# Performance work log

Measured on AMD Instinct MI355X. Metric: run time of the kernel, lower is better.

Reference implementation:

```python
import jax, jax.numpy as jnp
import numpy as np

H, W, SCALE = 480, 640, 8  # full-res grid and coarse downsample factor (hw0_i/hw0_c)


def _struct_feats(pts, anchor_ids):
    """pts: [N, H*W, 3]; anchor_ids: [N, A] int -> [N, L, 4*A] with L=(H//SCALE)*(W//SCALE)."""
    N = pts.shape[0]
    coarse = pts.reshape(N, H, W, 3)[:, ::SCALE, ::SCALE, :].reshape(N, -1, 3)  # [N, L, 3]
    anchors = jnp.take_along_axis(pts, anchor_ids[:, :, None], axis=1)          # [N, A, 3]
    diff = coarse[:, :, None, :] - anchors[:, None, :, :]                        # [N, L, A, 3]
    dist = jnp.sum(diff * diff, axis=-1, keepdims=True)                          # [N, L, A, 1]
    s = jnp.concatenate([diff, dist], axis=-1)                                   # [N, L, A, 4]
    s = s / jnp.sum(jnp.abs(s), axis=-2, keepdims=True)                          # L1 norm over anchor axis
    s = jnp.swapaxes(s, -1, -2).reshape(N, coarse.shape[1], -1)                  # [N, L, 4A]
    return s


def _mlp(x, W1, b1, W2, b2):
    return jax.nn.relu(x @ W1 + b1) @ W2 + b2


def setup_inputs() -> dict:
    key = jax.random.key(0)
    ks = jax.random.split(key, 10)
    N, L, C, A, P = 4, 4800, 256, 128, H * W
    D = C + 4 * A  # 768
    return {
        "feat0": jax.random.normal(ks[0], (N, L, C), jnp.float32),
        "feat1": jax.random.normal(ks[1], (N, L, C), jnp.float32),
        "pts_3d0": jax.random.normal(ks[2], (N, P, 3), jnp.float32),
        "pts_3d1": jax.random.normal(ks[3], (N, P, 3), jnp.float32),
        "anchor_i_ids": jax.random.randint(ks[4], (N, A), 0, P),
        "anchor_j_ids": jax.random.randint(ks[5], (N, A), 0, P),
        "W1": jax.random.normal(ks[6], (D, D), jnp.float32) * (1.0 / np.sqrt(D)),
        "b1": jnp.zeros((D,), jnp.float32),
        "W2": jax.random.normal(ks[7], (D, C), jnp.float32) * (1.0 / np.sqrt(D)),
        "b2": jnp.zeros((C,), jnp.float32),
    }


def reference(feat0, feat1, pts_3d0, pts_3d1, anchor_i_ids, anchor_j_ids, W1, b1, W2, b2):
    s0 = _struct_feats(pts_3d0, anchor_i_ids)  # [N, L, 4A]
    s1 = _struct_feats(pts_3d1, anchor_j_ids)
    aug0 = _mlp(jnp.concatenate([feat0, s0], axis=-1), W1, b1, W2, b2)  # [N, L, C]
    aug1 = _mlp(jnp.concatenate([feat1, s1], axis=-1), W1, b1, W2, b2)
    return (aug0, aug1)
```

## Files before the change

### kernel.cpp

```cpp
#include <hip/hip_runtime.h>
#include <stdint.h>
#include <stddef.h>

typedef __attribute__((ext_vector_type(8))) short short8;
typedef __attribute__((ext_vector_type(4))) short short4v;
typedef __attribute__((ext_vector_type(4))) float f32x4;

typedef const __attribute__((address_space(3))) char* lds_cp;

#define GLDS16(gp, lp)                                                        \
    __builtin_amdgcn_global_load_lds(                                         \
        (const __attribute__((address_space(1))) void*)(gp),                  \
        (__attribute__((address_space(3))) void*)(lp), 16, 0, 0)

__device__ __forceinline__ short8 ldsr16(lds_cp p) {
    short8 v;
    asm volatile("ds_read_b128 %0, %1" : "=v"(v) : "v"(p));
    return v;
}

template <int N>
__device__ __forceinline__ void wait_lgkm() {
    static_assert(N == 0 || N == 2 || N == 4 || N == 8, "unsupported count");
    if constexpr (N == 0) asm volatile("s_waitcnt lgkmcnt(0)" ::: "memory");
    else if constexpr (N == 2) asm volatile("s_waitcnt lgkmcnt(2)" ::: "memory");
    else if constexpr (N == 4) asm volatile("s_waitcnt lgkmcnt(4)" ::: "memory");
    else if constexpr (N == 8) asm volatile("s_waitcnt lgkmcnt(8)" ::: "memory");
    __builtin_amdgcn_sched_barrier(0);
}

template <int N>
__device__ __forceinline__ void wait_vm() {
    static_assert(N == 0 || N == 2 || N == 4, "unsupported count");
    if constexpr (N == 0) asm volatile("s_waitcnt vmcnt(0)" ::: "memory");
    else if constexpr (N == 2) asm volatile("s_waitcnt vmcnt(2)" ::: "memory");
    else if constexpr (N == 4) asm volatile("s_waitcnt vmcnt(4)" ::: "memory");
}

__device__ __forceinline__ unsigned short f2bf(float f) {
    union { float f; uint32_t u; } v;
    v.f = f;
    uint32_t u = v.u;
    u += 0x7FFFu + ((u >> 16) & 1u);
    return (unsigned short)(u >> 16);
}

__global__ __launch_bounds__(1024) void transpose_w(
    const float* __restrict__ W1, const float* __restrict__ W2,
    unsigned short* __restrict__ w1t, unsigned short* __restrict__ w2t)
{
    __shared__ float tile[32][33];
    int b = blockIdx.x;
    const float* src; unsigned short* dst; int R, C, bx, by;
    if (b < 576) { src = W1; dst = w1t; R = 768; C = 768; bx = b % 24; by = b / 24; }
    else { b -= 576; src = W2; dst = w2t; R = 768; C = 256; bx = b % 8; by = b / 8; }
    const int c0 = bx * 32, r0 = by * 32;
    const int tx = threadIdx.x, ty = threadIdx.y;
    tile[ty][tx] = src[(size_t)(r0 + ty) * C + (c0 + tx)];
    __syncthreads();
    dst[(size_t)(c0 + ty) * R + (r0 + tx)] = f2bf(tile[tx][ty]);
}

__global__ __launch_bounds__(256) void struct_pack(
    const float* __restrict__ feat0, const float* __restrict__ feat1,
    const float* __restrict__ pts0,  const float* __restrict__ pts1,
    const int* __restrict__ ids0,    const int* __restrict__ ids1,
    unsigned short* __restrict__ xw)
{
    const int m = blockIdx.x * 4 + (threadIdx.x >> 6);
    const int t = m / 19200;
    const int r = m % 19200;
    const int n = r / 4800;
    const int l = r % 4800;
    const float* feat = t ? feat1 : feat0;
    const float* pts  = (t ? pts1 : pts0) + (size_t)n * (307200 * 3);
    const int*   ids  = (t ? ids1 : ids0) + n * 128;
    const int a = threadIdx.x & 63;

    const int lr = l / 80, lc = l % 80;
    const int p  = (lr * 8) * 640 + lc * 8;
    const float cx = pts[p * 3 + 0], cy = pts[p * 3 + 1], cz = pts[p * 3 + 2];

    const int id0 = ids[a], id1 = ids[a + 64];
    const float d0x = cx - pts[id0 * 3 + 0];
    const float d0y = cy - pts[id0 * 3 + 1];
    const float d0z = cz - pts[id0 * 3 + 2];
    const float d0d = d0x * d0x + d0y * d0y + d0z * d0z;
    const float d1x = cx - pts[id1 * 3 + 0];
    const float d1y = cy - pts[id1 * 3 + 1];
    const float d1z = cz - pts[id1 * 3 + 2];
    const float d1d = d1x * d1x + d1y * d1y + d1z * d1z;

    float p0 = fabsf(d0x) + fabsf(d1x);
    float p1 = fabsf(d0y) + fabsf(d1y);
    float p2 = fabsf(d0z) + fabsf(d1z);
    float p3 = d0d + d1d;
#pragma unroll
    for (int off = 32; off; off >>= 1) {
        p0 += __shfl_xor(p0, off);
        p1 += __shfl_xor(p1, off);
        p2 += __shfl_xor(p2, off);
        p3 += __shfl_xor(p3, off);
    }
    const float i0 = 1.0f / p0, i1 = 1.0f / p1, i2 = 1.0f / p2, i3 = 1.0f / p3;

    unsigned short* xrow = xw + (size_t)m * 768;
    const float* frow = feat + (size_t)(n * 4800 + l) * 256;
    const float4 fv = ((const float4*)frow)[a];
    short4v s4;
    s4.x = (short)f2bf(fv.x); s4.y = (short)f2bf(fv.y);
    s4.z = (short)f2bf(fv.z); s4.w = (short)f2bf(fv.w);
    *(short4v*)(xrow + a * 4) = s4;

    xrow[256 + 0 * 128 + a]      = f2bf(d0x * i0);
    xrow[256 + 0 * 128 + a + 64] = f2bf(d1x * i0);
    xrow[256 + 1 * 128 + a]      = f2bf(d0y * i1);
    xrow[256 + 1 * 128 + a + 64] = f2bf(d1y * i1);
    xrow[256 + 2 * 128 + a]      = f2bf(d0z * i2);
    xrow[256 + 2 * 128 + a + 64] = f2bf(d1z * i2);
    xrow[256 + 3 * 128 + a]      = f2bf(d0d * i3);
    xrow[256 + 3 * 128 + a + 64] = f2bf(d1d * i3);
}

template <int MI, int NJ, int WRN_LOG, bool RELU, bool OUT_BF16>
__global__ __launch_bounds__(512, 2) void gemm_t(
    const unsigned short* __restrict__ A,
    const unsigned short* __restrict__ Bt,
    const float* __restrict__ bias,
    void* __restrict__ Cout,
    int K, int N, int ntx, int q8, int r8)
{
    constexpr int WRN = 1 << WRN_LOG;
    constexpr int WRM = 8 / WRN;
    constexpr int BM = WRM * MI * 16;
    constexpr int BN = WRN * NJ * 16;
    constexpr int ASLOT = BM * 128;
    constexpr int BSLOT = BN * 128;
    constexpr int ALD = BM / 64;
    constexpr int BLD = BN / 64;

    extern __shared__ char lds[];
    char* ldsB = lds + 3 * ASLOT;
    const int nt = K >> 6;

    const int bid = blockIdx.x;
    const int xcd = bid & 7, idx = bid >> 3;
    const int w = (xcd < r8 ? xcd * (q8 + 1) : r8 * (q8 + 1) + (xcd - r8) * q8) + idx;
    const int n0 = (w % ntx) * BN;
    const int m0 = (w / ntx) * BM;

    const int tid = threadIdx.x;
    const int lane = tid & 63;
    const int wv = tid >> 6;
    const int wr = wv >> WRN_LOG;
    const int wc = wv & (WRN - 1);

    const int slr = lane >> 3;
    const int kc  = (lane & 7) ^ slr;
    const unsigned short* gA = A  + (size_t)(m0 + wv * 8 + slr) * K + kc * 8;
    const unsigned short* gB = Bt + (size_t)(n0 + wv * 8 + slr) * K + kc * 8;

    auto stA = [&](int slot, int i, int kt) {
        GLDS16(gA + (size_t)i * 64 * K + kt, lds + slot * ASLOT + (i * 64 + wv * 8) * 128);
    };
    auto stB = [&](int slot, int j, int kt) {
        GLDS16(gB + (size_t)j * 64 * K + kt, ldsB + slot * BSLOT + (j * 64 + wv * 8) * 128);
    };

    const int rsel = lane & 15;
    const int kbh  = lane >> 4;
    const int ck0 = ((kbh) ^ (rsel & 7)) * 16;
    const int ck1 = ((4 + kbh) ^ (rsel & 7)) * 16;
    const int aRowB = (wr * (MI * 16) + rsel) * 128;
    const int bRowB = (wc * (NJ * 16) + rsel) * 128;

    auto LDA = [&](int slot, int mi, int ks) -> short8 {
        return ldsr16((lds_cp)(lds + slot * ASLOT + aRowB + mi * 2048 + (ks ? ck1 : ck0)));
    };
    auto LDB = [&](int slot, int nj, int ks) -> short8 {
        return ldsr16((lds_cp)(ldsB + slot * BSLOT + bRowB + nj * 2048 + (ks ? ck1 : ck0)));
    };

    f32x4 acc[MI][NJ] = {};
    short8 aL[MI / 2], aH[MI / 2], aL1[MI / 2], aH1[MI / 2], bF0[NJ], bF1[NJ];

    {
#pragma unroll
        for (int i = 0; i < ALD; ++i) stA(0, i, 0);
#pragma unroll
        for (int j = 0; j < BLD; ++j) stB(0, j, 0);
        if (nt > 1) {
#pragma unroll
            for (int i = 0; i < ALD; ++i) stA(1, i, 64);
            wait_vm<ALD>();
        } else {
            wait_vm<0>();
        }
        __builtin_amdgcn_s_barrier();
    }

    int cb3 = 0;
    for (int t = 0; t < nt; ++t) {
        const int cb2 = t & 1;
        const int sb2 = cb2 ^ 1;
        int sa3 = cb3 + 2; if (sa3 >= 3) sa3 -= 3;
        const int kt1 = (t + 1) << 6;
        const int kt2 = (t + 2) << 6;
        const bool stb = (t + 1) < nt;
        const bool sta = (t + 2) < nt;

#pragma unroll
        for (int nj = 0; nj < NJ; ++nj) bF0[nj] = LDB(cb2, nj, 0);
#pragma unroll
        for (int mi = 0; mi < MI / 2; ++mi) aL[mi] = LDA(cb3, mi, 0);
#pragma unroll
        for (int mi = 0; mi < MI / 2; ++mi) aH[mi] = LDA(cb3, MI / 2 + mi, 0);

        wait_lgkm<MI / 2>();
        __builtin_amdgcn_s_setprio(1);
#pragma unroll
        for (int mi = 0; mi < MI / 2; ++mi)
#pragma unroll
            for (int nj = 0; nj < NJ; ++nj)
                acc[mi][nj] = __builtin_amdgcn_mfma_f32_16x16x32_bf16(aL[mi], bF0[nj], acc[mi][nj], 0, 0, 0);
        __builtin_amdgcn_s_setprio(0);

#pragma unroll
        for (int nj = 0; nj < NJ; ++nj) bF1[nj] = LDB(cb2, nj, 1);
        if (stb) {
#pragma unroll
            for (int j = 0; j < BLD; ++j) stB(sb2, j, kt1);
        }

        wait_lgkm<NJ>();
        __builtin_amdgcn_s_setprio(1);
#pragma unroll
        for (int mi = 0; mi < MI / 2; ++mi)
#pragma unroll
            for (int nj = 0; nj < NJ; ++nj)
                acc[MI / 2 + mi][nj] = __builtin_amdgcn_mfma_f32_16x16x32_bf16(aH[mi], bF0[nj], acc[MI / 2 + mi][nj], 0, 0, 0);
        __builtin_amdgcn_s_setprio(0);

#pragma unroll
        for (int mi = 0; mi < MI / 2; ++mi) aL1[mi] = LDA(cb3, mi, 1);
#pragma unroll
        for (int mi = 0; mi < MI / 2; ++mi) aH1[mi] = LDA(cb3, MI / 2 + mi, 1);
        if (sta) {
#pragma unroll
            for (int i = 0; i < ALD; ++i) stA(sa3, i, kt2);
        }

        wait_lgkm<MI / 2>();
        __builtin_amdgcn_s_setprio(1);
#pragma unroll
        for (int mi = 0; mi < MI / 2; ++mi)
#pragma unroll
            for (int nj = 0; nj < NJ; ++nj)
                acc[mi][nj] = __builtin_amdgcn_mfma_f32_16x16x32_bf16(aL1[mi], bF1[nj], acc[mi][nj], 0, 0, 0);
        __builtin_amdgcn_s_setprio(0);

        wait_lgkm<0>();
        __builtin_amdgcn_s_setprio(1);
#pragma unroll
        for (int mi = 0; mi < MI / 2; ++mi)
#pragma unroll
            for (int nj = 0; nj < NJ; ++nj)
                acc[MI / 2 + mi][nj] = __builtin_amdgcn_mfma_f32_16x16x32_bf16(aH1[mi], bF1[nj], acc[MI / 2 + mi][nj], 0, 0, 0);
        __builtin_amdgcn_s_setprio(0);

        if (t + 1 < nt) {
            if (sta) wait_vm<ALD>();
            else     wait_vm<0>();
            __builtin_amdgcn_s_barrier();
        }
        cb3 = (cb3 + 1 == 3) ? 0 : cb3 + 1;
    }

    const int crow = (lane >> 4) * 4;
    const int ccol = lane & 15;
#pragma unroll
    for (int nj = 0; nj < NJ; ++nj) {
        const int col = n0 + wc * (NJ * 16) + nj * 16 + ccol;
        const float bv = bias[col];
#pragma unroll
        for (int mi = 0; mi < MI; ++mi) {
#pragma unroll
            for (int rg = 0; rg < 4; ++rg) {
                const int row = m0 + wr * (MI * 16) + mi * 16 + crow + rg;
                float v = acc[mi][nj][rg] + bv;
                if (RELU) v = fmaxf(v, 0.0f);
                if (OUT_BF16) {
                    ((unsigned short*)Cout)[(size_t)row * N + col] = f2bf(v);
                } else {
                    ((float*)Cout)[(size_t)row * N + col] = v;
                }
            }
        }
    }
}

extern "C" void kernel_launch(void* const* d_in, const int* in_sizes, int n_in,
                              void* d_out, int out_size, void* d_ws, size_t ws_size,
                              hipStream_t stream) {
    const float* feat0 = (const float*)d_in[0];
    const float* feat1 = (const float*)d_in[1];
    const float* pts0  = (const float*)d_in[2];
    const float* pts1  = (const float*)d_in[3];
    const int*   ids0  = (const int*)d_in[4];
    const int*   ids1  = (const int*)d_in[5];
    const float* W1    = (const float*)d_in[6];
    const float* b1    = (const float*)d_in[7];
    const float* W2    = (const float*)d_in[8];
    const float* b2    = (const float*)d_in[9];
    float* out = (float*)d_out;

    char* ws = (char*)d_ws;
    unsigned short* xw  = (unsigned short*)(ws);
    unsigned short* h   = (unsigned short*)(ws + 58982400);
    unsigned short* w1t = (unsigned short*)(ws + 117964800);
    unsigned short* w2t = (unsigned short*)(ws + 119144448);

    const int LDS1 = 3 * 32768 + 2 * 32768;
    const int LDS2 = 3 * 16384 + 2 * 16384;
    (void)hipFuncSetAttribute((const void*)&gemm_t<8, 4, 2, true, true>,
                              hipFuncAttributeMaxDynamicSharedMemorySize, LDS1);
    (void)hipFuncSetAttribute((const void*)&gemm_t<4, 2, 2, false, false>,
                              hipFuncAttributeMaxDynamicSharedMemorySize, LDS2);

    transpose_w<<<768, dim3(32, 32), 0, stream>>>(W1, W2, w1t, w2t);

    struct_pack<<<9600, 256, 0, stream>>>(feat0, feat1, pts0, pts1, ids0, ids1, xw);

    gemm_t<8, 4, 2, true, true><<<450, 512, LDS1, stream>>>(xw, w1t, b1, (void*)h, 768, 768, 3, 56, 2);
    gemm_t<4, 2, 2, false, false><<<600, 512, LDS2, stream>>>(h, w2t, b2, (void*)out, 768, 256, 2, 75, 0);
}
```

Baseline: 112.9 us.

## Add 256x128 pipelined GEMM kernel with A-fragment prefetch for first MLP layer

Replaces the first-layer GEMM (768x768 with ReLU and bf16 output) with a new kernel that uses 256x128 tiles instead of 256x256, doubling the grid to 900 blocks. The kernel keeps a three-stage global-to-LDS ring for both A and B and prefetches the next K-step's A fragments into registers while the current MFMAs run. LDS reads are interleaved with MFMA groups using fine-grained lgkmcnt waits and s_setprio. Smaller tiles cut per-block LDS and even out the work across CUs, at the cost of reloading A more often and holding more registers.

```diff
diff --git a/kernel.cpp b/kernel.cpp
--- a/kernel.cpp
+++ b/kernel.cpp
@@ -21,20 +21,22 @@
 
 template <int N>
 __device__ __forceinline__ void wait_lgkm() {
-    static_assert(N == 0 || N == 2 || N == 4 || N == 8, "unsupported count");
     if constexpr (N == 0) asm volatile("s_waitcnt lgkmcnt(0)" ::: "memory");
     else if constexpr (N == 2) asm volatile("s_waitcnt lgkmcnt(2)" ::: "memory");
     else if constexpr (N == 4) asm volatile("s_waitcnt lgkmcnt(4)" ::: "memory");
     else if constexpr (N == 8) asm volatile("s_waitcnt lgkmcnt(8)" ::: "memory");
+    else if constexpr (N == 10) asm volatile("s_waitcnt lgkmcnt(10)" ::: "memory");
+    else if constexpr (N == 12) asm volatile("s_waitcnt lgkmcnt(12)" ::: "memory");
+    else static_assert(N == 0, "unsupported count");
     __builtin_amdgcn_sched_barrier(0);
 }
 
 template <int N>
 __device__ __forceinline__ void wait_vm() {
-    static_assert(N == 0 || N == 2 || N == 4, "unsupported count");
     if constexpr (N == 0) asm volatile("s_waitcnt vmcnt(0)" ::: "memory");
     else if constexpr (N == 2) asm volatile("s_waitcnt vmcnt(2)" ::: "memory");
     else if constexpr (N == 4) asm volatile("s_waitcnt vmcnt(4)" ::: "memory");
+    else static_assert(N == 0, "unsupported count");
 }
 
 __device__ __forceinline__ unsigned short f2bf(float f) {
@@ -120,6 +122,202 @@
     xrow[256 + 2 * 128 + a + 64] = f2bf(d1z * i2);
     xrow[256 + 3 * 128 + a]      = f2bf(d0d * i3);
     xrow[256 + 3 * 128 + a + 64] = f2bf(d1d * i3);
+}
+
+template <bool RELU, bool OUT_BF16>
+__global__ __launch_bounds__(512, 2) void gemm_p(
+    const unsigned short* __restrict__ A,
+    const unsigned short* __restrict__ Bt,
+    const float* __restrict__ bias,
+    void* __restrict__ Cout,
+    int K, int N, int ntx, int q8, int r8)
+{
+    constexpr int ASLOT = 256 * 128;
+    constexpr int BSLOT = 128 * 128;
+    extern __shared__ char lds[];
+    char* ldsB = lds + 3 * ASLOT;
+    const int nt = K >> 6;
+
+    const int bid = blockIdx.x;
+    const int xcd = bid & 7, idx = bid >> 3;
+    const int w = (xcd < r8 ? xcd * (q8 + 1) : r8 * (q8 + 1) + (xcd - r8) * q8) + idx;
+    const int n0 = (w % ntx) * 128;
+    const int m0 = (w / ntx) * 256;
+
+    const int tid = threadIdx.x;
+    const int lane = tid & 63;
+    const int wv = tid >> 6;
+    const int wr = wv >> 1;
+    const int wc = wv & 1;
+
+    const int slr = lane >> 3;
+    const int kc  = (lane & 7) ^ slr;
+    const unsigned short* gA = A  + (size_t)(m0 + wv * 8 + slr) * K + kc * 8;
+    const unsigned short* gB = Bt + (size_t)(n0 + wv * 8 + slr) * K + kc * 8;
+
+    auto stA = [&](int slot, int i, int kt) {
+        GLDS16(gA + (size_t)i * 64 * K + kt, lds + slot * ASLOT + (i * 64 + wv * 8) * 128);
+    };
+    auto stB = [&](int slot, int j, int kt) {
+        GLDS16(gB + (size_t)j * 64 * K + kt, ldsB + slot * BSLOT + (j * 64 + wv * 8) * 128);
+    };
+
+    const int rsel = lane & 15;
+    const int kbh  = lane >> 4;
+    const int ck0 = ((kbh) ^ (rsel & 7)) * 16;
+    const int ck1 = ((4 + kbh) ^ (rsel & 7)) * 16;
+    const int aRowB = (wr * 64 + rsel) * 128;
+    const int bRowB = (wc * 64 + rsel) * 128;
+
+    auto LDA = [&](int slot, int mi, int ks) -> short8 {
+        return ldsr16((lds_cp)(lds + slot * ASLOT + aRowB + mi * 2048 + (ks ? ck1 : ck0)));
+    };
+    auto LDB = [&](int slot, int nj, int ks) -> short8 {
+        return ldsr16((lds_cp)(ldsB + slot * BSLOT + bRowB + nj * 2048 + (ks ? ck1 : ck0)));
+    };
+
+    f32x4 acc[4][4] = {};
+    short8 aF[4][2], aN[4][2], bP[4][2];
+
+    {
+        stB(0, 0, 0); stB(0, 1, 0);
+#pragma unroll
+        for (int i = 0; i < 4; ++i) stA(0, i, 0);
+        if (nt > 1) {
+            stB(1, 0, 64); stB(1, 1, 64);
+#pragma unroll
+            for (int i = 0; i < 4; ++i) stA(1, i, 64);
+        }
+        wait_vm<0>();
+        __builtin_amdgcn_s_barrier();
+#pragma unroll
+        for (int mi = 0; mi < 4; ++mi) {
+            aF[mi][0] = LDA(0, mi, 0);
+            aF[mi][1] = LDA(0, mi, 1);
+        }
+    }
+
+    int cur = 0;
+    for (int t = 0; t < nt - 1; ++t) {
+        int nxt = cur + 1; if (nxt == 3) nxt = 0;
+        int stg = nxt + 1; if (stg == 3) stg = 0;
+        const int kt2 = (t + 2) << 6;
+
+        if (t + 2 < nt) {
+            stB(stg, 0, kt2); stB(stg, 1, kt2);
+#pragma unroll
+            for (int i = 0; i < 4; ++i) stA(stg, i, kt2);
+        }
+
+        bP[0][0] = LDB(cur, 0, 0); bP[0][1] = LDB(cur, 0, 1);
+        bP[1][0] = LDB(cur, 1, 0); bP[1][1] = LDB(cur, 1, 1);
+        bP[2][0] = LDB(cur, 2, 0); bP[2][1] = LDB(cur, 2, 1);
+        aN[0][0] = LDA(nxt, 0, 0); aN[0][1] = LDA(nxt, 0, 1);
+        aN[1][0] = LDA(nxt, 1, 0); aN[1][1] = LDA(nxt, 1, 1);
+
+        wait_lgkm<8>();
+        __builtin_amdgcn_s_setprio(1);
+#pragma unroll
+        for (int mi = 0; mi < 4; ++mi)
+#pragma unroll
+            for (int ks = 0; ks < 2; ++ks)
+                acc[mi][0] = __builtin_amdgcn_mfma_f32_16x16x32_bf16(aF[mi][ks], bP[0][ks], acc[mi][0], 0, 0, 0);
+        __builtin_amdgcn_s_setprio(0);
+
+        bP[3][0] = LDB(cur, 3, 0); bP[3][1] = LDB(cur, 3, 1);
+        aN[2][0] = LDA(nxt, 2, 0); aN[2][1] = LDA(nxt, 2, 1);
+        aN[3][0] = LDA(nxt, 3, 0); aN[3][1] = LDA(nxt, 3, 1);
+
+        wait_lgkm<12>();
+        __builtin_amdgcn_s_setprio(1);
+#pragma unroll
+        for (int mi = 0; mi < 4; ++mi)
+#pragma unroll
+            for (int ks = 0; ks < 2; ++ks)
+                acc[mi][1] = __builtin_amdgcn_mfma_f32_16x16x32_bf16(aF[mi][ks], bP[1][ks], acc[mi][1], 0, 0, 0);
+        __builtin_amdgcn_s_setprio(0);
+
+        wait_lgkm<10>();
+        __builtin_amdgcn_s_setprio(1);
+#pragma unroll
+        for (int mi = 0; mi < 4; ++mi)
+#pragma unroll
+            for (int ks = 0; ks < 2; ++ks)
+                acc[mi][2] = __builtin_amdgcn_mfma_f32_16x16x32_bf16(aF[mi][ks], bP[2][ks], acc[mi][2], 0, 0, 0);
+        __builtin_amdgcn_s_setprio(0);
+
+        wait_lgkm<4>();
+        __builtin_amdgcn_s_setprio(1);
+#pragma unroll
+        for (int mi = 0; mi < 4; ++mi)
+#pragma unroll
+            for (int ks = 0; ks < 2; ++ks)
+                acc[mi][3] = __builtin_amdgcn_mfma_f32_16x16x32_bf16(aF[mi][ks], bP[3][ks], acc[mi][3], 0, 0, 0);
+        __builtin_amdgcn_s_setprio(0);
+
+#pragma unroll
+        for (int mi = 0; mi < 4; ++mi) {
+            aF[mi][0] = aN[mi][0];
+            aF[mi][1] = aN[mi][1];
+        }
+
+        wait_vm<0>();
+        __builtin_amdgcn_s_barrier();
+        cur = nxt;
+    }
+
+    {
+        bP[0][0] = LDB(cur, 0, 0); bP[0][1] = LDB(cur, 0, 1);
+        bP[1][0] = LDB(cur, 1, 0); bP[1][1] = LDB(cur, 1, 1);
+        bP[2][0] = LDB(cur, 2, 0); bP[2][1] = LDB(cur, 2, 1);
+        wait_lgkm<4>();
+#pragma unroll
+        for (int mi = 0; mi < 4; ++mi)
+#pragma unroll
+            for (int ks = 0; ks < 2; ++ks)
+                acc[mi][0] = __builtin_amdgcn_mfma_f32_16x16x32_bf16(aF[mi][ks], bP[0][ks], acc[mi][0], 0, 0, 0);
+        bP[3][0] = LDB(cur, 3, 0); bP[3][1] = LDB(cur, 3, 1);
+        wait_lgkm<4>();
+#pragma unroll
+        for (int mi = 0; mi < 4; ++mi)
+#pragma unroll
+            for (int ks = 0; ks < 2; ++ks)
+                acc[mi][1] = __builtin_amdgcn_mfma_f32_16x16x32_bf16(aF[mi][ks], bP[1][ks], acc[mi][1], 0, 0, 0);
+        wait_lgkm<2>();
+#pragma unroll
+        for (int mi = 0; mi < 4; ++mi)
+#pragma unroll
+            for (int ks = 0; ks < 2; ++ks)
+                acc[mi][2] = __builtin_amdgcn_mfma_f32_16x16x32_bf16(aF[mi][ks], bP[2][ks], acc[mi][2], 0, 0, 0);
+        wait_lgkm<0>();
+#pragma unroll
+        for (int mi = 0; mi < 4; ++mi)
+#pragma unroll
+            for (int ks = 0; ks < 2; ++ks)
+                acc[mi][3] = __builtin_amdgcn_mfma_f32_16x16x32_bf16(aF[mi][ks], bP[3][ks], acc[mi][3], 0, 0, 0);
+    }
+
+    const int crow = (lane >> 4) * 4;
+    const int ccol = lane & 15;
+#pragma unroll
+    for (int nj = 0; nj < 4; ++nj) {
+        const int col = n0 + wc * 64 + nj * 16 + ccol;
+        const float bv = bias[col];
+#pragma unroll
+        for (int mi = 0; mi < 4; ++mi) {
+#pragma unroll
+            for (int rg = 0; rg < 4; ++rg) {
+                const int row = m0 + wr * 64 + mi * 16 + crow + rg;
+                float v = acc[mi][nj][rg] + bv;
+                if (RELU) v = fmaxf(v, 0.0f);
+                if (OUT_BF16) {
+                    ((unsigned short*)Cout)[(size_t)row * N + col] = f2bf(v);
+                } else {
+                    ((float*)Cout)[(size_t)row * N + col] = v;
+                }
+            }
+        }
+    }
 }
 
 template <int MI, int NJ, int WRN_LOG, bool RELU, bool OUT_BF16>
@@ -320,9 +518,9 @@
     unsigned short* w1t = (unsigned short*)(ws + 117964800);
     unsigned short* w2t = (unsigned short*)(ws + 119144448);
 
-    const int LDS1 = 3 * 32768 + 2 * 32768;
+    const int LDS1 = 3 * 32768 + 3 * 16384;
     const int LDS2 = 3 * 16384 + 2 * 16384;
-    (void)hipFuncSetAttribute((const void*)&gemm_t<8, 4, 2, true, true>,
+    (void)hipFuncSetAttribute((const void*)&gemm_p<true, true>,
                               hipFuncAttributeMaxDynamicSharedMemorySize, LDS1);
     (void)hipFuncSetAttribute((const void*)&gemm_t<4, 2, 2, false, false>,
                               hipFuncAttributeMaxDynamicSharedMemorySize, LDS2);
@@ -331,6 +529,6 @@
 
     struct_pack<<<9600, 256, 0, stream>>>(feat0, feat1, pts0, pts1, ids0, ids1, xw);
 
-    gemm_t<8, 4, 2, true, true><<<450, 512, LDS1, stream>>>(xw, w1t, b1, (void*)h, 768, 768, 3, 56, 2);
+    gemm_p<true, true><<<900, 512, LDS1, stream>>>(xw, w1t, b1, (void*)h, 768, 768, 6, 112, 4);
     gemm_t<4, 2, 2, false, false><<<600, 512, LDS2, stream>>>(h, w2t, b2, (void*)out, 768, 256, 2, 75, 0);
 }
```

Measured after the change: 117.3 us. 3.9% more time.

## Merge weight transpose into prep kernel and stage GEMM1 bf16 epilogue through LDS

Applied to the files above, without the earlier changes.

The weight transpose/convert kernel and the struct-feature packing kernel become one launch, with extra blocks doing the 32x32 transposes using 256 threads. This removes one kernel launch and its inter-kernel gap. The first GEMM's bf16 epilogue now writes results into swizzled LDS and then stores full 16-byte row segments to global memory, replacing scattered 2-byte stores. In exchange it adds two block barriers and an LDS round trip in the epilogue.

```diff
diff --git a/kernel.cpp b/kernel.cpp
--- a/kernel.cpp
+++ b/kernel.cpp
@@ -21,20 +21,20 @@
 
 template <int N>
 __device__ __forceinline__ void wait_lgkm() {
-    static_assert(N == 0 || N == 2 || N == 4 || N == 8, "unsupported count");
     if constexpr (N == 0) asm volatile("s_waitcnt lgkmcnt(0)" ::: "memory");
     else if constexpr (N == 2) asm volatile("s_waitcnt lgkmcnt(2)" ::: "memory");
     else if constexpr (N == 4) asm volatile("s_waitcnt lgkmcnt(4)" ::: "memory");
     else if constexpr (N == 8) asm volatile("s_waitcnt lgkmcnt(8)" ::: "memory");
+    else static_assert(N == 0, "unsupported count");
     __builtin_amdgcn_sched_barrier(0);
 }
 
 template <int N>
 __device__ __forceinline__ void wait_vm() {
-    static_assert(N == 0 || N == 2 || N == 4, "unsupported count");
     if constexpr (N == 0) asm volatile("s_waitcnt vmcnt(0)" ::: "memory");
     else if constexpr (N == 2) asm volatile("s_waitcnt vmcnt(2)" ::: "memory");
     else if constexpr (N == 4) asm volatile("s_waitcnt vmcnt(4)" ::: "memory");
+    else static_assert(N == 0, "unsupported count");
 }
 
 __device__ __forceinline__ unsigned short f2bf(float f) {
@@ -45,81 +45,90 @@
     return (unsigned short)(u >> 16);
 }
 
-__global__ __launch_bounds__(1024) void transpose_w(
-    const float* __restrict__ W1, const float* __restrict__ W2,
+__global__ __launch_bounds__(256) void prep(
+    const float* __restrict__ feat0, const float* __restrict__ feat1,
+    const float* __restrict__ pts0,  const float* __restrict__ pts1,
+    const int* __restrict__ ids0,    const int* __restrict__ ids1,
+    const float* __restrict__ W1,    const float* __restrict__ W2,
+    unsigned short* __restrict__ xw,
     unsigned short* __restrict__ w1t, unsigned short* __restrict__ w2t)
 {
     __shared__ float tile[32][33];
     int b = blockIdx.x;
-    const float* src; unsigned short* dst; int R, C, bx, by;
-    if (b < 576) { src = W1; dst = w1t; R = 768; C = 768; bx = b % 24; by = b / 24; }
-    else { b -= 576; src = W2; dst = w2t; R = 768; C = 256; bx = b % 8; by = b / 8; }
-    const int c0 = bx * 32, r0 = by * 32;
-    const int tx = threadIdx.x, ty = threadIdx.y;
-    tile[ty][tx] = src[(size_t)(r0 + ty) * C + (c0 + tx)];
-    __syncthreads();
-    dst[(size_t)(c0 + ty) * R + (r0 + tx)] = f2bf(tile[tx][ty]);
-}
-
-__global__ __launch_bounds__(256) void struct_pack(
-    const float* __restrict__ feat0, const float* __restrict__ feat1,
-    const float* __restrict__ pts0,  const float* __restrict__ pts1,
-    const int* __restrict__ ids0,    const int* __restrict__ ids1,
-    unsigned short* __restrict__ xw)
-{
-    const int m = blockIdx.x * 4 + (threadIdx.x >> 6);
-    const int t = m / 19200;
-    const int r = m % 19200;
-    const int n = r / 4800;
-    const int l = r % 4800;
-    const float* feat = t ? feat1 : feat0;
-    const float* pts  = (t ? pts1 : pts0) + (size_t)n * (307200 * 3);
-    const int*   ids  = (t ? ids1 : ids0) + n * 128;
-    const int a = threadIdx.x & 63;
-
-    const int lr = l / 80, lc = l % 80;
-    const int p  = (lr * 8) * 640 + lc * 8;
-    const float cx = pts[p * 3 + 0], cy = pts[p * 3 + 1], cz = pts[p * 3 + 2];
-
-    const int id0 = ids[a], id1 = ids[a + 64];
-    const float d0x = cx - pts[id0 * 3 + 0];
-    const float d0y = cy - pts[id0 * 3 + 1];
-    const float d0z = cz - pts[id0 * 3 + 2];
-    const float d0d = d0x * d0x + d0y * d0y + d0z * d0z;
-    const float d1x = cx - pts[id1 * 3 + 0];
-    const float d1y = cy - pts[id1 * 3 + 1];
-    const float d1z = cz - pts[id1 * 3 + 2];
-    const float d1d = d1x * d1x + d1y * d1y + d1z * d1z;
-
-    float p0 = fabsf(d0x) + fabsf(d1x);
-    float p1 = fabsf(d0y) + fabsf(d1y);
-    float p2 = fabsf(d0z) + fabsf(d1z);
-    float p3 = d0d + d1d;
-#pragma unroll
-    for (int off = 32; off; off >>= 1) {
-        p0 += __shfl_xor(p0, off);
-        p1 += __shfl_xor(p1, off);
-        p2 += __shfl_xor(p2, off);
-        p3 += __shfl_xor(p3, off);
+    if (b < 9600) {
+        const int m = b * 4 + (threadIdx.x >> 6);
+        const int t = m / 19200;
+        const int r = m % 19200;
+        const int n = r / 4800;
+        const int l = r % 4800;
+        const float* feat = t ? feat1 : feat0;
+        const float* pts  = (t ? pts1 : pts0) + (size_t)n * (307200 * 3);
+        const int*   ids  = (t ? ids1 : ids0) + n * 128;
+        const int a = threadIdx.x & 63;
+
+        const int lr = l / 80, lc = l % 80;
+        const int p  = (lr * 8) * 640 + lc * 8;
+        const float cx = pts[p * 3 + 0], cy = pts[p * 3 + 1], cz = pts[p * 3 + 2];
+
+        const int id0 = ids[a], id1 = ids[a + 64];
+        const float d0x = cx - pts[id0 * 3 + 0];
+        const float d0y = cy - pts[id0 * 3 + 1];
+        const float d0z = cz - pts[id0 * 3 + 2];
+        const float d0d = d0x * d0x + d0y * d0y + d0z * d0z;
+        const float d1x = cx - pts[id1 * 3 + 0];
+        const float d1y = cy - pts[id1 * 3 + 1];
+        const float d1z = cz - pts[id1 * 3 + 2];
+        const float d1d = d1x * d1x + d1y * d1y + d1z * d1z;
+
+        float p0 = fabsf(d0x) + fabsf(d1x);
+        float p1 = fabsf(d0y) + fabsf(d1y);
+        float p2 = fabsf(d0z) + fabsf(d1z);
+        float p3 = d0d + d1d;
+#pragma unroll
+        for (int off = 32; off; off >>= 1) {
+            p0 += __shfl_xor(p0, off);
+            p1 += __shfl_xor(p1, off);
+            p2 += __shfl_xor(p2, off);
+            p3 += __shfl_xor(p3, off);
+        }
+        const float i0 = 1.0f / p0, i1 = 1.0f / p1, i2 = 1.0f / p2, i3 = 1.0f / p3;
+
+        unsigned short* xrow = xw + (size_t)m * 768;
+        const float* frow = feat + (size_t)(n * 4800 + l) * 256;
+        const float4 fv = ((const float4*)frow)[a];
+        short4v s4;
+        s4.x = (short)f2bf(fv.x); s4.y = (short)f2bf(fv.y);
+        s4.z = (short)f2bf(fv.z); s4.w = (short)f2bf(fv.w);
+        *(short4v*)(xrow + a * 4) = s4;
+
+        xrow[256 + 0 * 128 + a]      = f2bf(d0x * i0);
+        xrow[256 + 0 * 128 + a + 64] = f2bf(d1x * i0);
+        xrow[256 + 1 * 128 + a]      = f2bf(d0y * i1);
+        xrow[256 + 1 * 128 + a + 64] = f2bf(d1y * i1);
+        xrow[256 + 2 * 128 + a]      = f2bf(d0z * i2);
+        xrow[256 + 2 * 128 + a + 64] = f2bf(d1z * i2);
+        xrow[256 + 3 * 128 + a]      = f2bf(d0d * i3);
+        xrow[256 + 3 * 128 + a + 64] = f2bf(d1d * i3);
+    } else {
+        b -= 9600;
+        const float* src; unsigned short* dst; int C, bx, by;
+        if (b < 576) { src = W1; dst = w1t; C = 768; bx = b % 24; by = b / 24; }
+        else { b -= 576; src = W2; dst = w2t; C = 256; bx = b % 8; by = b / 8; }
+        const int R = 768;
+        const int c0 = bx * 32, r0 = by * 32;
+        const int tx = threadIdx.x & 31, ty0 = threadIdx.x >> 5;
+#pragma unroll
+        for (int rr = 0; rr < 4; ++rr) {
+            const int ty = ty0 * 4 + rr;
+            tile[ty][tx] = src[(size_t)(r0 + ty) * C + (c0 + tx)];
+        }
+        __syncthreads();
+#pragma unroll
+        for (int rr = 0; rr < 4; ++rr) {
+            const int ty = ty0 * 4 + rr;
+            dst[(size_t)(c0 + ty) * R + (r0 + tx)] = f2bf(tile[tx][ty]);
+        }
     }
-    const float i0 = 1.0f / p0, i1 = 1.0f / p1, i2 = 1.0f / p2, i3 = 1.0f / p3;
-
-    unsigned short* xrow = xw + (size_t)m * 768;
-    const float* frow = feat + (size_t)(n * 4800 + l) * 256;
-    const float4 fv = ((const float4*)frow)[a];
-    short4v s4;
-    s4.x = (short)f2bf(fv.x); s4.y = (short)f2bf(fv.y);
-    s4.z = (short)f2bf(fv.z); s4.w = (short)f2bf(fv.w);
-    *(short4v*)(xrow + a * 4) = s4;
-
-    xrow[256 + 0 * 128 + a]      = f2bf(d0x * i0);
-    xrow[256 + 0 * 128 + a + 64] = f2bf(d1x * i0);
-    xrow[256 + 1 * 128 + a]      = f2bf(d0y * i1);
-    xrow[256 + 1 * 128 + a + 64] = f2bf(d1y * i1);
-    xrow[256 + 2 * 128 + a]      = f2bf(d0z * i2);
-    xrow[256 + 2 * 128 + a + 64] = f2bf(d1z * i2);
-    xrow[256 + 3 * 128 + a]      = f2bf(d0d * i3);
-    xrow[256 + 3 * 128 + a + 64] = f2bf(d1d * i3);
 }
 
 template <int MI, int NJ, int WRN_LOG, bool RELU, bool OUT_BF16>
@@ -278,21 +287,57 @@
 
     const int crow = (lane >> 4) * 4;
     const int ccol = lane & 15;
-#pragma unroll
-    for (int nj = 0; nj < NJ; ++nj) {
-        const int col = n0 + wc * (NJ * 16) + nj * 16 + ccol;
-        const float bv = bias[col];
-#pragma unroll
-        for (int mi = 0; mi < MI; ++mi) {
-#pragma unroll
-            for (int rg = 0; rg < 4; ++rg) {
-                const int row = m0 + wr * (MI * 16) + mi * 16 + crow + rg;
-                float v = acc[mi][nj][rg] + bv;
-                if (RELU) v = fmaxf(v, 0.0f);
-                if (OUT_BF16) {
-                    ((unsigned short*)Cout)[(size_t)row * N + col] = f2bf(v);
-                } else {
-                    ((float*)Cout)[(size_t)row * N + col] = v;
+
+    if constexpr (OUT_BF16 && BM == 256) {
+        __syncthreads();
+        unsigned short* cl = (unsigned short*)lds;
+#pragma unroll
+        for (int nj = 0; nj < NJ; ++nj) {
+            const int col = wc * (NJ * 16) + nj * 16 + ccol;
+            const float bv = bias[n0 + col];
+            const int c = col >> 3;
+#pragma unroll
+            for (int mi = 0; mi < MI; ++mi) {
+#pragma unroll
+                for (int rg = 0; rg < 4; ++rg) {
+                    const int row = wr * (MI * 16) + mi * 16 + crow + rg;
+                    float v = acc[mi][nj][rg] + bv;
+                    if (RELU) v = fmaxf(v, 0.0f);
+                    const int pc = (c & ~7) | ((c ^ row) & 7);
+                    cl[row * BN + pc * 8 + (col & 7)] = f2bf(v);
+                }
+            }
+        }
+        __syncthreads();
+#pragma unroll
+        for (int h2 = 0; h2 < 2; ++h2) {
+            const int rrow = wv * 32 + h2 * 16 + (lane >> 2);
+            unsigned short* outp = (unsigned short*)Cout + (size_t)(m0 + rrow) * N + n0;
+#pragma unroll
+            for (int s = 0; s < BN / 32; ++s) {
+                const int c = s * 4 + (lane & 3);
+                const int pc = (c & ~7) | ((c ^ rrow) & 7);
+                short8 vv = *(const short8*)&cl[rrow * BN + pc * 8];
+                *(short8*)(outp + c * 8) = vv;
+            }
+        }
+    } else {
+#pragma unroll
+        for (int nj = 0; nj < NJ; ++nj) {
+            const int col = n0 + wc * (NJ * 16) + nj * 16 + ccol;
+            const float bv = bias[col];
+#pragma unroll
+            for (int mi = 0; mi < MI; ++mi) {
+#pragma unroll
+                for (int rg = 0; rg < 4; ++rg) {
+                    const int row = m0 + wr * (MI * 16) + mi * 16 + crow + rg;
+                    float v = acc[mi][nj][rg] + bv;
+                    if (RELU) v = fmaxf(v, 0.0f);
+                    if (OUT_BF16) {
+                        ((unsigned short*)Cout)[(size_t)row * N + col] = f2bf(v);
+                    } else {
+                        ((float*)Cout)[(size_t)row * N + col] = v;
+                    }
                 }
             }
         }
@@ -327,9 +372,8 @@
     (void)hipFuncSetAttribute((const void*)&gemm_t<4, 2, 2, false, false>,
                               hipFuncAttributeMaxDynamicSharedMemorySize, LDS2);
 
-    transpose_w<<<768, dim3(32, 32), 0, stream>>>(W1, W2, w1t, w2t);
-
-    struct_pack<<<9600, 256, 0, stream>>>(feat0, feat1, pts0, pts1, ids0, ids1, xw);
+    prep<<<10368, 256, 0, stream>>>(feat0, feat1, pts0, pts1, ids0, ids1,
+                                    W1, W2, xw, w1t, w2t);
 
     gemm_t<8, 4, 2, true, true><<<450, 512, LDS1, stream>>>(xw, w1t, b1, (void*)h, 768, 768, 3, 56, 2);
     gemm_t<4, 2, 2, false, false><<<600, 512, LDS2, stream>>>(h, w2t, b2, (void*)out, 768, 256, 2, 75, 0);
```

Measured after the change: 105.2 us (median of 2 runs). 1.07x faster.
